# Kernel tuning notes

Measured on AMD Instinct MI355X. Metric: run time of the kernel, lower is better.

## Reference

```python
import jax, jax.numpy as jnp
import numpy as np

EPS = 1e-10

def setup_inputs() -> dict:
    key = jax.random.key(0)
    k1, k2 = jax.random.split(key)
    support_set = jax.random.normal(k1, (8192, 1024), dtype=jnp.float32)
    input_image = jax.random.normal(k2, (2048, 1024), dtype=jnp.float32)
    return {"support_set": support_set, "input_image": input_image}

def reference(support_set, input_image):
    # support_set: [n, d], input_image: [b, d]
    # Faithful to original: input magnitude is a single scalar over the whole
    # [b, d] input matrix; support magnitude is a scalar per support vector.
    input_mag = jax.lax.rsqrt(jnp.maximum(jnp.sum(input_image * input_image), EPS))  # scalar
    support_mag = jax.lax.rsqrt(jnp.maximum(jnp.sum(support_set * support_set, axis=1), EPS))  # [n]
    dot = jnp.einsum('bd,nd->nb', input_image, support_set)  # [n, b]
    sims = dot * support_mag[:, None] * input_mag  # [n, b]
    return sims[:, :, None]  # [n, b, 1] == torch.stack(...)[n,b,1].squeeze(1) (no-op for b>1)
```

## Files before the change

kernel.cpp:

```cpp
#include <hip/hip_runtime.h>
#include <hip/hip_bf16.h>
#include <stdint.h>
#include <stddef.h>

#define M_DIM 8192
#define N_DIM 2048
#define K_DIM 1024

#define BM 128
#define BN 128
#define BK 64

typedef __attribute__((ext_vector_type(8))) short short8;
typedef __attribute__((ext_vector_type(4))) float float4v;

static __device__ __forceinline__ unsigned short f2bf(float x) {
  union { float f; unsigned u; } c; c.f = x;
  return (unsigned short)((c.u + 0x7FFFu + ((c.u >> 16) & 1u)) >> 16);
}

#define GLOAD_LDS16(g, l)                                           \
  __builtin_amdgcn_global_load_lds(                                 \
      (const __attribute__((address_space(1))) void*)(g),           \
      (__attribute__((address_space(3))) void*)(l), 16, 0, 0)


__global__ __launch_bounds__(256) void support_prep(
    const float* __restrict__ S, unsigned short* __restrict__ Sb,
    float* __restrict__ smag) {
  const int row = blockIdx.x;
  const int t = threadIdx.x;
  const float4 v = reinterpret_cast<const float4*>(S + (size_t)row * K_DIM)[t];
  ushort4 b;
  b.x = f2bf(v.x); b.y = f2bf(v.y); b.z = f2bf(v.z); b.w = f2bf(v.w);
  reinterpret_cast<ushort4*>(Sb + (size_t)row * K_DIM)[t] = b;

  float ss = v.x * v.x + v.y * v.y + v.z * v.z + v.w * v.w;
#pragma unroll
  for (int m = 32; m >= 1; m >>= 1) ss += __shfl_xor(ss, m, 64);
  __shared__ float wsum[4];
  if ((t & 63) == 0) wsum[t >> 6] = ss;
  __syncthreads();
  if (t == 0) smag[row] = rsqrtf(fmaxf(wsum[0] + wsum[1] + wsum[2] + wsum[3], 1e-10f));
}

__global__ __launch_bounds__(256) void input_prep(
    const float* __restrict__ I, unsigned short* __restrict__ Ib,
    float* __restrict__ partials) {
  const int idx = blockIdx.x * 256 + threadIdx.x;
  const float4 v = reinterpret_cast<const float4*>(I)[idx];
  ushort4 b;
  b.x = f2bf(v.x); b.y = f2bf(v.y); b.z = f2bf(v.z); b.w = f2bf(v.w);
  reinterpret_cast<ushort4*>(Ib)[idx] = b;

  float ss = v.x * v.x + v.y * v.y + v.z * v.z + v.w * v.w;
#pragma unroll
  for (int m = 32; m >= 1; m >>= 1) ss += __shfl_xor(ss, m, 64);
  __shared__ float wsum[4];
  const int t = threadIdx.x;
  if ((t & 63) == 0) wsum[t >> 6] = ss;
  __syncthreads();
  if (t == 0) partials[blockIdx.x] = wsum[0] + wsum[1] + wsum[2] + wsum[3];
}

__global__ __launch_bounds__(256) void finalize(
    const float* __restrict__ partials, const float* __restrict__ smag,
    float* __restrict__ scale) {
  const int t = threadIdx.x;
  float s = 0.f;
#pragma unroll
  for (int i = 0; i < 2048 / 256; ++i) s += partials[t + i * 256];
#pragma unroll
  for (int m = 32; m >= 1; m >>= 1) s += __shfl_xor(s, m, 64);
  __shared__ float wsum[4];
  if ((t & 63) == 0) wsum[t >> 6] = s;
  __syncthreads();
  const float imag = rsqrtf(fmaxf(wsum[0] + wsum[1] + wsum[2] + wsum[3], 1e-10f));
  for (int i = t; i < M_DIM; i += 256) scale[i] = smag[i] * imag;
}

__global__ __launch_bounds__(256) void gemm_bt(
    const unsigned short* __restrict__ A,
    const unsigned short* __restrict__ B,
    const float* __restrict__ scale,
    float* __restrict__ C) {
  __shared__ unsigned short lA[BM * BK];
  __shared__ unsigned short lB[BN * BK];

  const int t = threadIdx.x;
  const int lane = t & 63;
  const int wave = t >> 6;
  const int wr = wave >> 1;
  const int wc = wave & 1;

  const int bm = blockIdx.y * BM;
  const int bn = blockIdx.x * BN;

  const int rsub = lane >> 3;
  const int kcg = (lane & 7) ^ (rsub & 7);
  const unsigned short* gA[4];
  const unsigned short* gB[4];
  unsigned short* dA[4];
  unsigned short* dB[4];
#pragma unroll
  for (int i = 0; i < 4; ++i) {
    const int row = i * 32 + wave * 8 + rsub;
    gA[i] = A + (size_t)(bm + row) * K_DIM + kcg * 8;
    gB[i] = B + (size_t)(bn + row) * K_DIM + kcg * 8;
    dA[i] = lA + (size_t)(i * 256 + wave * 64) * 8;
    dB[i] = lB + (size_t)(i * 256 + wave * 64) * 8;
  }

  const int fr = lane & 15;
  const int q = lane >> 4;
  const unsigned short* rA = lA + (wr * 64 + fr) * BK;
  const unsigned short* rB = lB + (wc * 64 + fr) * BK;
  const int sw = fr & 7;

  float4v acc[4][4];
#pragma unroll
  for (int i = 0; i < 4; ++i)
#pragma unroll
    for (int j = 0; j < 4; ++j) acc[i][j] = (float4v)0.0f;

  for (int kt = 0; kt < K_DIM / BK; ++kt) {
#pragma unroll
    for (int i = 0; i < 4; ++i) GLOAD_LDS16(gA[i], dA[i]);
#pragma unroll
    for (int i = 0; i < 4; ++i) GLOAD_LDS16(gB[i], dB[i]);
#pragma unroll
    for (int i = 0; i < 4; ++i) { gA[i] += BK; gB[i] += BK; }
    __syncthreads();

#pragma unroll
    for (int s = 0; s < 2; ++s) {
      const int pc = ((4 * s + q) ^ sw) * 8;
      short8 af[4], bfr[4];
#pragma unroll
      for (int i = 0; i < 4; ++i)
        af[i] = *reinterpret_cast<const short8*>(rA + i * 16 * BK + pc);
#pragma unroll
      for (int j = 0; j < 4; ++j)
        bfr[j] = *reinterpret_cast<const short8*>(rB + j * 16 * BK + pc);
#pragma unroll
      for (int i = 0; i < 4; ++i)
#pragma unroll
        for (int j = 0; j < 4; ++j)
          acc[i][j] = __builtin_amdgcn_mfma_f32_16x16x32_bf16(af[i], bfr[j], acc[i][j], 0, 0, 0);
    }
    __syncthreads();
  }

#pragma unroll
  for (int i = 0; i < 4; ++i) {
    const int rbase = bm + wr * 64 + i * 16 + q * 4;
#pragma unroll
    for (int r = 0; r < 4; ++r) {
      const int row = rbase + r;
      const float s = scale[row];
      float* crow = C + (size_t)row * N_DIM + bn + wc * 64 + fr;
#pragma unroll
      for (int j = 0; j < 4; ++j) crow[j * 16] = acc[i][j][r] * s;
    }
  }
}

extern "C" void kernel_launch(void* const* d_in, const int* in_sizes, int n_in,
                              void* d_out, int out_size, void* d_ws, size_t ws_size,
                              hipStream_t stream) {
  const float* S = (const float*)d_in[0];
  const float* I = (const float*)d_in[1];
  float* out = (float*)d_out;

  unsigned char* ws = (unsigned char*)d_ws;
  unsigned short* Sb = (unsigned short*)ws;
  unsigned short* Ib = (unsigned short*)(ws + (size_t)M_DIM * K_DIM * 2);
  float* smag = (float*)(ws + (size_t)M_DIM * K_DIM * 2 + (size_t)N_DIM * K_DIM * 2);
  float* partials = smag + M_DIM;
  float* scale = partials + 2048;

  hipLaunchKernelGGL(input_prep, dim3((N_DIM * K_DIM) / (256 * 4)), dim3(256), 0, stream,
                     I, Ib, partials);
  hipLaunchKernelGGL(support_prep, dim3(M_DIM), dim3(256), 0, stream, S, Sb, smag);
  hipLaunchKernelGGL(finalize, dim3(1), dim3(256), 0, stream, partials, smag, scale);
  hipLaunchKernelGGL(gemm_bt, dim3(N_DIM / BN, M_DIM / BM), dim3(256), 0, stream,
                     Sb, Ib, scale, out);
}
```

Before: 142.4 us.

## Merge prep kernels, fold scale finalize into GEMM, remap blocks per XCD

Merges the support and input conversion kernels into one launch with one block per row. The single-block finalize kernel is dropped: each GEMM block now reduces the 2048 input partials itself and applies smag times imag in the epilogue. The GEMM grid becomes 1D with a mapping that gives each XCD (blk&7) a contiguous group of 8 M-tiles, aiming for better L2 reuse. This removes two launches and a serial single-block stage, at the cost of every GEMM block redundantly reading 8 KB of partials.

```diff
diff --git a/kernel.cpp b/kernel.cpp
--- a/kernel.cpp
+++ b/kernel.cpp
@@ -24,16 +24,21 @@
       (const __attribute__((address_space(1))) void*)(g),           \
       (__attribute__((address_space(3))) void*)(l), 16, 0, 0)
 
+__global__ __launch_bounds__(256) void prep(
+    const float* __restrict__ S, const float* __restrict__ I,
+    unsigned short* __restrict__ Sb, unsigned short* __restrict__ Ib,
+    float* __restrict__ smag, float* __restrict__ partials) {
+  const int t = threadIdx.x;
+  const int blk = blockIdx.x;
+  const bool isS = blk < M_DIM;
+  const int row = isS ? blk : blk - M_DIM;
+  const float* src = (isS ? S : I) + (size_t)row * K_DIM;
+  unsigned short* dst = (isS ? Sb : Ib) + (size_t)row * K_DIM;
 
-__global__ __launch_bounds__(256) void support_prep(
-    const float* __restrict__ S, unsigned short* __restrict__ Sb,
-    float* __restrict__ smag) {
-  const int row = blockIdx.x;
-  const int t = threadIdx.x;
-  const float4 v = reinterpret_cast<const float4*>(S + (size_t)row * K_DIM)[t];
+  const float4 v = reinterpret_cast<const float4*>(src)[t];
   ushort4 b;
   b.x = f2bf(v.x); b.y = f2bf(v.y); b.z = f2bf(v.z); b.w = f2bf(v.w);
-  reinterpret_cast<ushort4*>(Sb + (size_t)row * K_DIM)[t] = b;
+  reinterpret_cast<ushort4*>(dst)[t] = b;
 
   float ss = v.x * v.x + v.y * v.y + v.z * v.z + v.w * v.w;
 #pragma unroll
@@ -41,51 +46,22 @@
   __shared__ float wsum[4];
   if ((t & 63) == 0) wsum[t >> 6] = ss;
   __syncthreads();
-  if (t == 0) smag[row] = rsqrtf(fmaxf(wsum[0] + wsum[1] + wsum[2] + wsum[3], 1e-10f));
-}
-
-__global__ __launch_bounds__(256) void input_prep(
-    const float* __restrict__ I, unsigned short* __restrict__ Ib,
-    float* __restrict__ partials) {
-  const int idx = blockIdx.x * 256 + threadIdx.x;
-  const float4 v = reinterpret_cast<const float4*>(I)[idx];
-  ushort4 b;
-  b.x = f2bf(v.x); b.y = f2bf(v.y); b.z = f2bf(v.z); b.w = f2bf(v.w);
-  reinterpret_cast<ushort4*>(Ib)[idx] = b;
-
-  float ss = v.x * v.x + v.y * v.y + v.z * v.z + v.w * v.w;
-#pragma unroll
-  for (int m = 32; m >= 1; m >>= 1) ss += __shfl_xor(ss, m, 64);
-  __shared__ float wsum[4];
-  const int t = threadIdx.x;
-  if ((t & 63) == 0) wsum[t >> 6] = ss;
-  __syncthreads();
-  if (t == 0) partials[blockIdx.x] = wsum[0] + wsum[1] + wsum[2] + wsum[3];
-}
-
-__global__ __launch_bounds__(256) void finalize(
-    const float* __restrict__ partials, const float* __restrict__ smag,
-    float* __restrict__ scale) {
-  const int t = threadIdx.x;
-  float s = 0.f;
-#pragma unroll
-  for (int i = 0; i < 2048 / 256; ++i) s += partials[t + i * 256];
-#pragma unroll
-  for (int m = 32; m >= 1; m >>= 1) s += __shfl_xor(s, m, 64);
-  __shared__ float wsum[4];
-  if ((t & 63) == 0) wsum[t >> 6] = s;
-  __syncthreads();
-  const float imag = rsqrtf(fmaxf(wsum[0] + wsum[1] + wsum[2] + wsum[3], 1e-10f));
-  for (int i = t; i < M_DIM; i += 256) scale[i] = smag[i] * imag;
+  if (t == 0) {
+    const float tot = wsum[0] + wsum[1] + wsum[2] + wsum[3];
+    if (isS) smag[row] = rsqrtf(fmaxf(tot, 1e-10f));
+    else     partials[row] = tot;
+  }
 }
 
 __global__ __launch_bounds__(256) void gemm_bt(
     const unsigned short* __restrict__ A,
     const unsigned short* __restrict__ B,
-    const float* __restrict__ scale,
+    const float* __restrict__ smag,
+    const float* __restrict__ partials,
     float* __restrict__ C) {
   __shared__ unsigned short lA[BM * BK];
   __shared__ unsigned short lB[BN * BK];
+  __shared__ float wsum[4];
 
   const int t = threadIdx.x;
   const int lane = t & 63;
@@ -93,8 +69,20 @@
   const int wr = wave >> 1;
   const int wc = wave & 1;
 
-  const int bm = blockIdx.y * BM;
-  const int bn = blockIdx.x * BN;
+  const int blk = blockIdx.x;
+  const int xcd = blk & 7;
+  const int slot = blk >> 3;
+  const int bn = (slot >> 3) * BN;
+  const int bm = (xcd * 8 + (slot & 7)) * BM;
+
+  {
+    float p = 0.f;
+#pragma unroll
+    for (int i = 0; i < 2048 / 256; ++i) p += partials[t + i * 256];
+#pragma unroll
+    for (int m = 32; m >= 1; m >>= 1) p += __shfl_xor(p, m, 64);
+    if ((t & 63) == 0) wsum[t >> 6] = p;
+  }
 
   const int rsub = lane >> 3;
   const int kcg = (lane & 7) ^ (rsub & 7);
@@ -151,13 +139,14 @@
     __syncthreads();
   }
 
+  const float imag = rsqrtf(fmaxf(wsum[0] + wsum[1] + wsum[2] + wsum[3], 1e-10f));
 #pragma unroll
   for (int i = 0; i < 4; ++i) {
     const int rbase = bm + wr * 64 + i * 16 + q * 4;
 #pragma unroll
     for (int r = 0; r < 4; ++r) {
       const int row = rbase + r;
-      const float s = scale[row];
+      const float s = smag[row] * imag;
       float* crow = C + (size_t)row * N_DIM + bn + wc * 64 + fr;
 #pragma unroll
       for (int j = 0; j < 4; ++j) crow[j * 16] = acc[i][j][r] * s;
@@ -177,12 +166,9 @@
   unsigned short* Ib = (unsigned short*)(ws + (size_t)M_DIM * K_DIM * 2);
   float* smag = (float*)(ws + (size_t)M_DIM * K_DIM * 2 + (size_t)N_DIM * K_DIM * 2);
   float* partials = smag + M_DIM;
-  float* scale = partials + 2048;
 
-  hipLaunchKernelGGL(input_prep, dim3((N_DIM * K_DIM) / (256 * 4)), dim3(256), 0, stream,
-                     I, Ib, partials);
-  hipLaunchKernelGGL(support_prep, dim3(M_DIM), dim3(256), 0, stream, S, Sb, smag);
-  hipLaunchKernelGGL(finalize, dim3(1), dim3(256), 0, stream, partials, smag, scale);
-  hipLaunchKernelGGL(gemm_bt, dim3(N_DIM / BN, M_DIM / BM), dim3(256), 0, stream,
-                     Sb, Ib, scale, out);
+  hipLaunchKernelGGL(prep, dim3(M_DIM + N_DIM), dim3(256), 0, stream,
+                     S, I, Sb, Ib, smag, partials);
+  hipLaunchKernelGGL(gemm_bt, dim3((M_DIM / BM) * (N_DIM / BN)), dim3(256), 0, stream,
+                     Sb, Ib, smag, partials, out);
 }
```

Result: faster. 134.7 us (-5.4%).
